# Kernel tuning notes

Hardware: AMD Instinct MI355X
Metric: run time of the kernel (lower is better)

Reference implementation:

```python
import jax, jax.numpy as jnp
import numpy as np

D_QK = 32  # out_channels // 8


def conv1x1(x, w, b):
    # x: [B,C,H,W], w: [O,C], b: [O] -> [B,O,H,W]
    return jnp.einsum('bchw,oc->bohw', x, w) + b[None, :, None, None]


def setup_inputs() -> dict:
    key = jax.random.key(0)
    ks = jax.random.split(key, 10)
    B, C, H, W = 4, 256, 64, 64
    in_ch, out_ch, attn_ch = 512, 256, 256
    s_in = 1.0 / np.sqrt(in_ch)
    s_at = 1.0 / np.sqrt(attn_ch)
    return {
        'ef': jax.random.normal(ks[0], (B, C, H, W), jnp.float32),
        'sf': jax.random.normal(ks[1], (B, C, H, W), jnp.float32),
        'Attn': jax.random.normal(ks[2], (B, attn_ch, H, W), jnp.float32),
        'Qw': jax.random.uniform(ks[3], (D_QK, in_ch), jnp.float32, -s_in, s_in),
        'Qb': jax.random.uniform(ks[4], (D_QK,), jnp.float32, -s_in, s_in),
        'Kw': jax.random.uniform(ks[5], (D_QK, attn_ch), jnp.float32, -s_at, s_at),
        'Kb': jax.random.uniform(ks[6], (D_QK,), jnp.float32, -s_at, s_at),
        'Vw': jax.random.uniform(ks[7], (out_ch, in_ch), jnp.float32, -s_in, s_in),
        'Vb': jax.random.uniform(ks[8], (out_ch,), jnp.float32, -s_in, s_in),
        'gamma': jnp.ones((1,), jnp.float32) * 0.25,
    }


def reference(ef, sf, Attn, Qw, Qb, Kw, Kb, Vw, Vb, gamma):
    B, C, H, W = ef.shape
    N = H * W
    x = jnp.concatenate((ef, sf), axis=1)  # [B, 2C, H, W]
    q = conv1x1(x, Qw, Qb).reshape(B, D_QK, N)         # [B, d, N]
    k = conv1x1(Attn, Kw, Kb).reshape(B, D_QK, N)      # [B, d, N]
    # scores[b, m, n] = sum_d q[b, d, m] * k[b, d, n]  (no 1/sqrt(d) scale)
    scores = jnp.einsum('bdm,bdn->bmn', q, k)
    attn = jax.nn.softmax(scores, axis=-1)             # [B, N, N]
    v = conv1x1(x, Vw, Vb).reshape(B, C, N)            # [B, C, N]
    # out[b, c, m] = sum_n v[b, c, n] * attn[b, m, n]
    out = jnp.einsum('bcn,bmn->bcm', v, attn).reshape(B, C, H, W)
    return gamma[0] * out + ef
```

## Files before the change

### kernel.cpp

```cpp
#include <hip/hip_runtime.h>
#include <hip/hip_bf16.h>

typedef short bf16x8 __attribute__((ext_vector_type(8)));
typedef float f32x4 __attribute__((ext_vector_type(4)));

#define MFMA16(a, b, c) __builtin_amdgcn_mfma_f32_16x16x32_bf16(a, b, c, 0, 0, 0)

#define NB 4
#define NC 256
#define NSP 4096
#define LOG2E 1.4426950408889634f

__device__ __forceinline__ unsigned short f2bf(float f) {
    return (unsigned short)((__float_as_uint(f) + 0x8000u) >> 16);
}
__device__ __forceinline__ unsigned pk2bf(float hi, float lo) {
    return __builtin_amdgcn_perm(__float_as_uint(hi) + 0x8000u,
                                 __float_as_uint(lo) + 0x8000u, 0x07060302u);
}

__global__ __launch_bounds__(256) void prep_w(
    const float* __restrict__ Qw, const float* __restrict__ Kw,
    const float* __restrict__ Vw,
    unsigned short* __restrict__ Qwbf, unsigned short* __restrict__ Kwbf,
    unsigned short* __restrict__ Vwbf)
{
    int i = blockIdx.x * 256 + threadIdx.x;
    {
        const float4* vs = (const float4*)(Vw + (size_t)i * 8);
        float4 a = vs[0], c = vs[1];
        int4 st;
        st.x = (int)pk2bf(a.y, a.x); st.y = (int)pk2bf(a.w, a.z);
        st.z = (int)pk2bf(c.y, c.x); st.w = (int)pk2bf(c.w, c.z);
        *(int4*)(Vwbf + (size_t)i * 8) = st;
    }
    if (i < 2048) {
        const float4* qs = (const float4*)(Qw + (size_t)i * 8);
        float4 a = qs[0], c = qs[1];
        int4 st;
        st.x = (int)pk2bf(a.y, a.x); st.y = (int)pk2bf(a.w, a.z);
        st.z = (int)pk2bf(c.y, c.x); st.w = (int)pk2bf(c.w, c.z);
        *(int4*)(Qwbf + (size_t)i * 8) = st;
    }
    if (i < 1024) {
        const float4* ks = (const float4*)(Kw + (size_t)i * 8);
        float4 a = ks[0], c = ks[1];
        int4 st;
        st.x = (int)pk2bf(a.y, a.x); st.y = (int)pk2bf(a.w, a.z);
        st.z = (int)pk2bf(c.y, c.x); st.w = (int)pk2bf(c.w, c.z);
        *(int4*)(Kwbf + (size_t)i * 8) = st;
    }
}

__global__ __launch_bounds__(256, 2) void proj_qv(
    const float* __restrict__ ef, const float* __restrict__ sf,
    const unsigned short* __restrict__ Qwbf, const float* __restrict__ Qb,
    const unsigned short* __restrict__ Vwbf, const float* __restrict__ Vb,
    unsigned short* __restrict__ qws, unsigned short* __restrict__ vws)
{
    __shared__ __align__(16) unsigned short xt[2][32][72];

    int t = threadIdx.x;
    int w = t >> 6, lane = t & 63, quad = lane >> 4, l15 = lane & 15;
    int mt = blockIdx.x, b = blockIdx.y, m0 = mt * 32;
    int u = t & 7, v = t >> 3;
    int mi = w >> 1, oh = w & 1;

    float4 xA[8], xB[8];
#pragma unroll
    for (int c = 0; c < 8; ++c) {
        const float* sp = (c < 4 ? ef : sf) +
                          ((size_t)(b * NC) + (c & 3) * 64 + 2 * v) * NSP + m0 + u * 4;
        xA[c] = *(const float4*)sp;
        xB[c] = *(const float4*)(sp + NSP);
    }

    f32x4 zero = {0.f, 0.f, 0.f, 0.f};
    f32x4 acc[2][4];
#pragma unroll
    for (int m = 0; m < 2; ++m)
#pragma unroll
        for (int ot = 0; ot < 4; ++ot) acc[m][ot] = zero;
    f32x4 qacc = zero;

#pragma unroll
    for (int c = 0; c < 8; ++c) {
        unsigned* xw = (unsigned*)&xt[c & 1][u * 4][2 * v];
        xw[0]   = pk2bf(xB[c].x, xA[c].x);
        xw[36]  = pk2bf(xB[c].y, xA[c].y);
        xw[72]  = pk2bf(xB[c].z, xA[c].z);
        xw[108] = pk2bf(xB[c].w, xA[c].w);
        __syncthreads();
        int ci0 = c * 64;
#pragma unroll
        for (int ks = 0; ks < 2; ++ks) {
            bf16x8 a0 = *(const bf16x8*)&xt[c & 1][l15][ks * 32 + quad * 8];
            bf16x8 a1 = *(const bf16x8*)&xt[c & 1][16 + l15][ks * 32 + quad * 8];
            bf16x8 bq = *(const bf16x8*)(Qwbf + (size_t)(oh * 16 + l15) * 512 + ci0 + ks * 32 + quad * 8);
            qacc = MFMA16(mi ? a1 : a0, bq, qacc);
#pragma unroll
            for (int ot = 0; ot < 4; ++ot) {
                bf16x8 bv = *(const bf16x8*)(Vwbf + (size_t)(w * 64 + ot * 16 + l15) * 512 + ci0 + ks * 32 + quad * 8);
                acc[0][ot] = MFMA16(a0, bv, acc[0][ot]);
                acc[1][ot] = MFMA16(a1, bv, acc[1][ot]);
            }
        }
    }

#pragma unroll
    for (int ot = 0; ot < 4; ++ot) {
        int ch = w * 64 + ot * 16 + l15;
        float bias = Vb[ch];
        unsigned* vp = (unsigned*)(vws + ((size_t)((b * 128 + mt) * 256 + ch)) * 32);
#pragma unroll
        for (int r = 0; r < 4; ++r)
            vp[quad * 4 + r] = pk2bf(acc[1][ot][r] + bias, acc[0][ot][r] + bias);
    }

    {
        int o = oh * 16 + l15;
        float bb = Qb[o];
#pragma unroll
        for (int r = 0; r < 4; ++r) {
            int m = m0 + mi * 16 + quad * 4 + r;
            qws[((size_t)(b * NSP) + m) * 32 + o] = f2bf((qacc[r] + bb) * LOG2E);
        }
    }
}

__global__ __launch_bounds__(256, 2) void proj_k(
    const float* __restrict__ attn,
    const unsigned short* __restrict__ Kwbf, const float* __restrict__ Kb,
    unsigned short* __restrict__ kws)
{
    __shared__ __align__(16) unsigned short xt[2][32][72];

    int t = threadIdx.x;
    int w = t >> 6, lane = t & 63, quad = lane >> 4, l15 = lane & 15;
    int mt = blockIdx.x, b = blockIdx.y, m0 = mt * 32;
    int u = t & 7, v = t >> 3;
    int mi = w >> 1, oh = w & 1;

    float4 xA[4], xB[4];
#pragma unroll
    for (int c = 0; c < 4; ++c) {
        const float* sp = attn + ((size_t)(b * NC) + c * 64 + 2 * v) * NSP + m0 + u * 4;
        xA[c] = *(const float4*)sp;
        xB[c] = *(const float4*)(sp + NSP);
    }

    f32x4 acc = {0.f, 0.f, 0.f, 0.f};

#pragma unroll
    for (int c = 0; c < 4; ++c) {
        unsigned* xw = (unsigned*)&xt[c & 1][u * 4][2 * v];
        xw[0]   = pk2bf(xB[c].x, xA[c].x);
        xw[36]  = pk2bf(xB[c].y, xA[c].y);
        xw[72]  = pk2bf(xB[c].z, xA[c].z);
        xw[108] = pk2bf(xB[c].w, xA[c].w);
        __syncthreads();
        int ci0 = c * 64;
#pragma unroll
        for (int ks = 0; ks < 2; ++ks) {
            bf16x8 a  = *(const bf16x8*)&xt[c & 1][mi * 16 + l15][ks * 32 + quad * 8];
            bf16x8 bk = *(const bf16x8*)(Kwbf + (size_t)(oh * 16 + l15) * 256 + ci0 + ks * 32 + quad * 8);
            acc = MFMA16(a, bk, acc);
        }
    }

    int o = oh * 16 + l15;
    float bb = Kb[o];
#pragma unroll
    for (int r = 0; r < 4; ++r) {
        int m = m0 + mi * 16 + quad * 4 + r;
        kws[((size_t)(b * NSP) + m) * 32 + o] = f2bf(acc[r] + bb);
    }
}

#define ATT_ITER(IT, VCUR, VNXT)                                              \
    {                                                                         \
        int buf = (IT) & 1;                                                   \
        f32x4 s0 = MFMA16(qf, kf[0], zero);                                   \
        f32x4 s1 = MFMA16(qf, kf[1], zero);                                   \
        f32x4 s2 = MFMA16(qf, kf[2], zero);                                   \
        f32x4 s3 = MFMA16(qf, kf[3], zero);                                   \
        float e0[4], e1[4], e2[4], e3[4];                                     \
        _Pragma("unroll")                                                     \
        for (int r = 0; r < 4; ++r) {                                         \
            e0[r] = __builtin_amdgcn_exp2f(s0[r]);                            \
            e1[r] = __builtin_amdgcn_exp2f(s1[r]);                            \
            e2[r] = __builtin_amdgcn_exp2f(s2[r]);                            \
            e3[r] = __builtin_amdgcn_exp2f(s3[r]);                            \
        }                                                                     \
        lp0 += (e0[0] + e1[0]) + (e2[0] + e3[0]);                             \
        lp1 += (e0[1] + e1[1]) + (e2[1] + e3[1]);                             \
        lp2 += (e0[2] + e1[2]) + (e2[2] + e3[2]);                             \
        lp3 += (e0[3] + e1[3]) + (e2[3] + e3[3]);                             \
        unsigned short* pd = &Plds[g][buf][(w * 16 + quad * 4) * 72 + 2 * l15]; \
        _Pragma("unroll")                                                     \
        for (int r = 0; r < 4; ++r) {                                         \
            *(unsigned*)(pd + r * 72)      = pk2bf(e1[r], e0[r]);             \
            *(unsigned*)(pd + r * 72 + 32) = pk2bf(e3[r], e2[r]);             \
        }                                                                     \
        int itn = (IT) + 1 < 32 ? (IT) + 1 : 31;                              \
        int ttn = tt0 + 2 * itn;                                              \
        _Pragma("unroll")                                                     \
        for (int j = 0; j < 4; ++j)                                           \
            kf[j] = *(const bf16x8*)(kbase + (size_t)((ttn + (j >> 1)) * 32 + (j & 1) * 16 + l15) * 32 + quad * 8); \
        _Pragma("unroll")                                                     \
        for (int h = 0; h < 2; ++h)                                           \
            _Pragma("unroll")                                                 \
            for (int cc = 0; cc < 4; ++cc)                                    \
                VNXT[h][cc] = *(const bf16x8*)(vbase + (size_t)(ttn + h) * 8192 + (w * 64 + cc * 16 + l15) * 32 + quad * 8); \
        __syncthreads();                                                      \
        _Pragma("unroll")                                                     \
        for (int h = 0; h < 2; ++h) {                                         \
            bf16x8 pa0 = *(const bf16x8*)&Plds[g][buf][(0  + l15) * 72 + h * 32 + quad * 8]; \
            bf16x8 pa1 = *(const bf16x8*)&Plds[g][buf][(16 + l15) * 72 + h * 32 + quad * 8]; \
            bf16x8 pa2 = *(const bf16x8*)&Plds[g][buf][(32 + l15) * 72 + h * 32 + quad * 8]; \
            bf16x8 pa3 = *(const bf16x8*)&Plds[g][buf][(48 + l15) * 72 + h * 32 + quad * 8]; \
            _Pragma("unroll")                                                 \
            for (int cc = 0; cc < 4; ++cc) {                                  \
                acc[0][cc] = MFMA16(pa0, VCUR[h][cc], acc[0][cc]);            \
                acc[1][cc] = MFMA16(pa1, VCUR[h][cc], acc[1][cc]);            \
                acc[2][cc] = MFMA16(pa2, VCUR[h][cc], acc[2][cc]);            \
                acc[3][cc] = MFMA16(pa3, VCUR[h][cc], acc[3][cc]);            \
            }                                                                 \
        }                                                                     \
    }

__global__ __launch_bounds__(512, 2) void attention(
    const unsigned short* __restrict__ qws, const unsigned short* __restrict__ kws,
    const unsigned short* __restrict__ vws, const float* __restrict__ ef,
    const float* __restrict__ gamma, float* __restrict__ out)
{
    __shared__ unsigned short Plds[2][2][64 * 72];
    __shared__ float mrg[256][68];
    __shared__ float denl[2][64];

    int t = threadIdx.x;
    int g = t >> 8, tl = t & 255;
    int w = tl >> 6, lane = tl & 63, quad = lane >> 4, l15 = lane & 15;
    int b = blockIdx.x >> 6, m0 = (blockIdx.x & 63) << 6;

    const unsigned short* kbase = kws + (size_t)(b * NSP) * 32;
    const unsigned short* vbase = vws + (size_t)(b * 128) * 8192;

    bf16x8 qf = *(const bf16x8*)(qws + ((size_t)(b * NSP) + m0 + w * 16 + l15) * 32 + quad * 8);

    f32x4 zero = {0.f, 0.f, 0.f, 0.f};
    f32x4 acc[4][4];
#pragma unroll
    for (int i = 0; i < 4; ++i)
#pragma unroll
        for (int j = 0; j < 4; ++j) acc[i][j] = zero;
    float lp0 = 0.f, lp1 = 0.f, lp2 = 0.f, lp3 = 0.f;

    int tt0 = g * 64;
    bf16x8 kf[4];
#pragma unroll
    for (int j = 0; j < 4; ++j)
        kf[j] = *(const bf16x8*)(kbase + (size_t)((tt0 + (j >> 1)) * 32 + (j & 1) * 16 + l15) * 32 + quad * 8);
    bf16x8 vfA[2][4], vfB[2][4];
#pragma unroll
    for (int h = 0; h < 2; ++h)
#pragma unroll
        for (int cc = 0; cc < 4; ++cc)
            vfA[h][cc] = *(const bf16x8*)(vbase + (size_t)(tt0 + h) * 8192 + (w * 64 + cc * 16 + l15) * 32 + quad * 8);

    for (int it2 = 0; it2 < 16; ++it2) {
        ATT_ITER(2 * it2,     vfA, vfB);
        ATT_ITER(2 * it2 + 1, vfB, vfA);
    }

    lp0 += __shfl_xor(lp0, 1); lp0 += __shfl_xor(lp0, 2); lp0 += __shfl_xor(lp0, 4); lp0 += __shfl_xor(lp0, 8);
    lp1 += __shfl_xor(lp1, 1); lp1 += __shfl_xor(lp1, 2); lp1 += __shfl_xor(lp1, 4); lp1 += __shfl_xor(lp1, 8);
    lp2 += __shfl_xor(lp2, 1); lp2 += __shfl_xor(lp2, 2); lp2 += __shfl_xor(lp2, 4); lp2 += __shfl_xor(lp2, 8);
    lp3 += __shfl_xor(lp3, 1); lp3 += __shfl_xor(lp3, 2); lp3 += __shfl_xor(lp3, 4); lp3 += __shfl_xor(lp3, 8);
    if (l15 == 0) {
        int base = w * 16 + quad * 4;
        denl[g][base + 0] = lp0; denl[g][base + 1] = lp1;
        denl[g][base + 2] = lp2; denl[g][base + 3] = lp3;
    }
    if (g == 1) {
#pragma unroll
        for (int qc = 0; qc < 4; ++qc)
#pragma unroll
            for (int cc = 0; cc < 4; ++cc)
                *(f32x4*)&mrg[w * 64 + cc * 16 + l15][qc * 16 + quad * 4] = acc[qc][cc];
    }
    __syncthreads();

    if (g == 0) {
        float gam = gamma[0];
#pragma unroll
        for (int qc = 0; qc < 4; ++qc) {
            int qb = qc * 16 + quad * 4;
            float4 d0 = *(const float4*)&denl[0][qb];
            float4 d1 = *(const float4*)&denl[1][qb];
            float r0 = gam / (d0.x + d1.x), r1 = gam / (d0.y + d1.y);
            float r2 = gam / (d0.z + d1.z), r3 = gam / (d0.w + d1.w);
#pragma unroll
            for (int cc = 0; cc < 4; ++cc) {
                int ch = w * 64 + cc * 16 + l15;
                f32x4 part = *(const f32x4*)&mrg[ch][qb];
                size_t off = ((size_t)(b * NC + ch)) * NSP + m0 + qb;
                float4 e = *(const float4*)(ef + off);
                float4 o;
                o.x = (acc[qc][cc][0] + part[0]) * r0 + e.x;
                o.y = (acc[qc][cc][1] + part[1]) * r1 + e.y;
                o.z = (acc[qc][cc][2] + part[2]) * r2 + e.z;
                o.w = (acc[qc][cc][3] + part[3]) * r3 + e.w;
                *(float4*)(out + off) = o;
            }
        }
    }
}

extern "C" void kernel_launch(void* const* d_in, const int* in_sizes, int n_in,
                              void* d_out, int out_size, void* d_ws, size_t ws_size,
                              hipStream_t stream) {
    const float* ef    = (const float*)d_in[0];
    const float* sf    = (const float*)d_in[1];
    const float* attn  = (const float*)d_in[2];
    const float* Qw    = (const float*)d_in[3];
    const float* Qb    = (const float*)d_in[4];
    const float* Kw    = (const float*)d_in[5];
    const float* Kb    = (const float*)d_in[6];
    const float* Vw    = (const float*)d_in[7];
    const float* Vb    = (const float*)d_in[8];
    const float* gamma = (const float*)d_in[9];
    float* out = (float*)d_out;

    unsigned short* qws  = (unsigned short*)d_ws;
    unsigned short* kws  = qws + (size_t)4 * 4096 * 32;
    unsigned short* vws  = kws + (size_t)4 * 4096 * 32;
    unsigned short* Qwbf = vws + (size_t)4 * 128 * 256 * 32;
    unsigned short* Kwbf = Qwbf + 32 * 512;
    unsigned short* Vwbf = Kwbf + 32 * 256;

    hipLaunchKernelGGL(prep_w, dim3(64), dim3(256), 0, stream,
                       Qw, Kw, Vw, Qwbf, Kwbf, Vwbf);
    hipLaunchKernelGGL(proj_qv, dim3(128, 4), dim3(256), 0, stream,
                       ef, sf, Qwbf, Qb, Vwbf, Vb, qws, vws);
    hipLaunchKernelGGL(proj_k, dim3(128, 4), dim3(256), 0, stream,
                       attn, Kwbf, Kb, kws);
    hipLaunchKernelGGL(attention, dim3(256), dim3(512), 0, stream,
                       qws, kws, vws, ef, gamma, out);
}
```

Measured before the change: 179.8 us.

## Split attention key range into separate blocks with global merge kernel

Replaces the single 512-thread attention kernel, which split the key range between two thread groups inside one block and merged through shared memory, with 512 independent 256-thread blocks that each handle half of the keys. Each block writes unnormalised partial outputs and denominators to global memory, and a new elementwise kernel sums the two halves, normalises, applies gamma and adds the residual. This aims to raise occupancy and drop the large shared-memory merge buffer. In exchange it adds about 16 MB of extra global traffic and one more launch. Scheduling barriers are also added after the input loads in the projection kernels.

```diff
diff --git a/kernel.cpp b/kernel.cpp
--- a/kernel.cpp
+++ b/kernel.cpp
@@ -74,6 +74,7 @@
         xA[c] = *(const float4*)sp;
         xB[c] = *(const float4*)(sp + NSP);
     }
+    __builtin_amdgcn_sched_barrier(0);
 
     f32x4 zero = {0.f, 0.f, 0.f, 0.f};
     f32x4 acc[2][4];
@@ -116,7 +117,6 @@
         for (int r = 0; r < 4; ++r)
             vp[quad * 4 + r] = pk2bf(acc[1][ot][r] + bias, acc[0][ot][r] + bias);
     }
-
     {
         int o = oh * 16 + l15;
         float bb = Qb[o];
@@ -148,6 +148,7 @@
         xA[c] = *(const float4*)sp;
         xB[c] = *(const float4*)(sp + NSP);
     }
+    __builtin_amdgcn_sched_barrier(0);
 
     f32x4 acc = {0.f, 0.f, 0.f, 0.f};
 
@@ -175,6 +176,148 @@
         int m = m0 + mi * 16 + quad * 4 + r;
         kws[((size_t)(b * NSP) + m) * 32 + o] = f2bf(acc[r] + bb);
     }
+}
+
+#define ATT_ITER_P(IT, VCUR, VNXT)                                            \
+    {                                                                         \
+        int buf = (IT) & 1;                                                   \
+        f32x4 s0 = MFMA16(qf, kf[0], zero);                                   \
+        f32x4 s1 = MFMA16(qf, kf[1], zero);                                   \
+        f32x4 s2 = MFMA16(qf, kf[2], zero);                                   \
+        f32x4 s3 = MFMA16(qf, kf[3], zero);                                   \
+        float e0[4], e1[4], e2[4], e3[4];                                     \
+        _Pragma("unroll")                                                     \
+        for (int r = 0; r < 4; ++r) {                                         \
+            e0[r] = __builtin_amdgcn_exp2f(s0[r]);                            \
+            e1[r] = __builtin_amdgcn_exp2f(s1[r]);                            \
+            e2[r] = __builtin_amdgcn_exp2f(s2[r]);                            \
+            e3[r] = __builtin_amdgcn_exp2f(s3[r]);                            \
+        }                                                                     \
+        lp0 += (e0[0] + e1[0]) + (e2[0] + e3[0]);                             \
+        lp1 += (e0[1] + e1[1]) + (e2[1] + e3[1]);                             \
+        lp2 += (e0[2] + e1[2]) + (e2[2] + e3[2]);                             \
+        lp3 += (e0[3] + e1[3]) + (e2[3] + e3[3]);                             \
+        unsigned short* pd = &Plds[buf][(w * 16 + quad * 4) * 72 + 2 * l15];  \
+        _Pragma("unroll")                                                     \
+        for (int r = 0; r < 4; ++r) {                                         \
+            *(unsigned*)(pd + r * 72)      = pk2bf(e1[r], e0[r]);             \
+            *(unsigned*)(pd + r * 72 + 32) = pk2bf(e3[r], e2[r]);             \
+        }                                                                     \
+        int itn = (IT) + 1 < 32 ? (IT) + 1 : 31;                              \
+        int ttn = tt0 + 2 * itn;                                              \
+        _Pragma("unroll")                                                     \
+        for (int j = 0; j < 4; ++j)                                           \
+            kf[j] = *(const bf16x8*)(kbase + (size_t)((ttn + (j >> 1)) * 32 + (j & 1) * 16 + l15) * 32 + quad * 8); \
+        _Pragma("unroll")                                                     \
+        for (int h = 0; h < 2; ++h)                                           \
+            _Pragma("unroll")                                                 \
+            for (int cc = 0; cc < 4; ++cc)                                    \
+                VNXT[h][cc] = *(const bf16x8*)(vbase + (size_t)(ttn + h) * 8192 + (w * 64 + cc * 16 + l15) * 32 + quad * 8); \
+        __syncthreads();                                                      \
+        _Pragma("unroll")                                                     \
+        for (int h = 0; h < 2; ++h) {                                         \
+            bf16x8 pa0 = *(const bf16x8*)&Plds[buf][(0  + l15) * 72 + h * 32 + quad * 8]; \
+            bf16x8 pa1 = *(const bf16x8*)&Plds[buf][(16 + l15) * 72 + h * 32 + quad * 8]; \
+            bf16x8 pa2 = *(const bf16x8*)&Plds[buf][(32 + l15) * 72 + h * 32 + quad * 8]; \
+            bf16x8 pa3 = *(const bf16x8*)&Plds[buf][(48 + l15) * 72 + h * 32 + quad * 8]; \
+            _Pragma("unroll")                                                 \
+            for (int cc = 0; cc < 4; ++cc) {                                  \
+                acc[0][cc] = MFMA16(pa0, VCUR[h][cc], acc[0][cc]);            \
+                acc[1][cc] = MFMA16(pa1, VCUR[h][cc], acc[1][cc]);            \
+                acc[2][cc] = MFMA16(pa2, VCUR[h][cc], acc[2][cc]);            \
+                acc[3][cc] = MFMA16(pa3, VCUR[h][cc], acc[3][cc]);            \
+            }                                                                 \
+        }                                                                     \
+    }
+
+__global__ __launch_bounds__(256, 2) void attention_part(
+    const unsigned short* __restrict__ qws, const unsigned short* __restrict__ kws,
+    const unsigned short* __restrict__ vws,
+    float* __restrict__ opart0, float* __restrict__ opart1,
+    float* __restrict__ denp)
+{
+    __shared__ unsigned short Plds[2][64 * 72];
+
+    int t = threadIdx.x;
+    int w = t >> 6, lane = t & 63, quad = lane >> 4, l15 = lane & 15;
+    int bx = blockIdx.x;
+    int g = bx & 1;
+    int r2 = bx >> 1;
+    int b = r2 >> 6, m0 = (r2 & 63) << 6;
+
+    const unsigned short* kbase = kws + (size_t)(b * NSP) * 32;
+    const unsigned short* vbase = vws + (size_t)(b * 128) * 8192;
+
+    bf16x8 qf = *(const bf16x8*)(qws + ((size_t)(b * NSP) + m0 + w * 16 + l15) * 32 + quad * 8);
+
+    f32x4 zero = {0.f, 0.f, 0.f, 0.f};
+    f32x4 acc[4][4];
+#pragma unroll
+    for (int i = 0; i < 4; ++i)
+#pragma unroll
+        for (int j = 0; j < 4; ++j) acc[i][j] = zero;
+    float lp0 = 0.f, lp1 = 0.f, lp2 = 0.f, lp3 = 0.f;
+
+    int tt0 = g * 64;
+    bf16x8 kf[4];
+#pragma unroll
+    for (int j = 0; j < 4; ++j)
+        kf[j] = *(const bf16x8*)(kbase + (size_t)((tt0 + (j >> 1)) * 32 + (j & 1) * 16 + l15) * 32 + quad * 8);
+    bf16x8 vfA[2][4], vfB[2][4];
+#pragma unroll
+    for (int h = 0; h < 2; ++h)
+#pragma unroll
+        for (int cc = 0; cc < 4; ++cc)
+            vfA[h][cc] = *(const bf16x8*)(vbase + (size_t)(tt0 + h) * 8192 + (w * 64 + cc * 16 + l15) * 32 + quad * 8);
+
+    for (int it2 = 0; it2 < 16; ++it2) {
+        ATT_ITER_P(2 * it2,     vfA, vfB);
+        ATT_ITER_P(2 * it2 + 1, vfB, vfA);
+    }
+
+    lp0 += __shfl_xor(lp0, 1); lp0 += __shfl_xor(lp0, 2); lp0 += __shfl_xor(lp0, 4); lp0 += __shfl_xor(lp0, 8);
+    lp1 += __shfl_xor(lp1, 1); lp1 += __shfl_xor(lp1, 2); lp1 += __shfl_xor(lp1, 4); lp1 += __shfl_xor(lp1, 8);
+    lp2 += __shfl_xor(lp2, 1); lp2 += __shfl_xor(lp2, 2); lp2 += __shfl_xor(lp2, 4); lp2 += __shfl_xor(lp2, 8);
+    lp3 += __shfl_xor(lp3, 1); lp3 += __shfl_xor(lp3, 2); lp3 += __shfl_xor(lp3, 4); lp3 += __shfl_xor(lp3, 8);
+    if (l15 == 0) {
+        float* dp = denp + ((size_t)(g * 4 + b)) * NSP + m0 + w * 16 + quad * 4;
+        dp[0] = lp0; dp[1] = lp1; dp[2] = lp2; dp[3] = lp3;
+    }
+
+    float* od = g ? opart1 : opart0;
+#pragma unroll
+    for (int qc = 0; qc < 4; ++qc) {
+#pragma unroll
+        for (int cc = 0; cc < 4; ++cc) {
+            int ch = w * 64 + cc * 16 + l15;
+            size_t off = ((size_t)(b * NC + ch)) * NSP + m0 + qc * 16 + quad * 4;
+            *(f32x4*)(od + off) = acc[qc][cc];
+        }
+    }
+}
+
+__global__ __launch_bounds__(256) void attn_merge(
+    const float* __restrict__ o1, const float* __restrict__ denp,
+    const float* __restrict__ ef, const float* __restrict__ gamma,
+    float* __restrict__ out)
+{
+    size_t i = (size_t)blockIdx.x * 256 + threadIdx.x;
+    size_t off = i * 4;
+    int m = (int)(off & (NSP - 1));
+    int b = (int)(i >> 18);
+
+    float4 a0 = *(const float4*)(out + off);
+    float4 a1 = *(const float4*)(o1 + off);
+    float4 d0 = *(const float4*)(denp + ((size_t)(0 * 4 + b)) * NSP + m);
+    float4 d1 = *(const float4*)(denp + ((size_t)(1 * 4 + b)) * NSP + m);
+    float4 e  = *(const float4*)(ef + off);
+    float gam = gamma[0];
+    float4 o;
+    o.x = (a0.x + a1.x) * (gam / (d0.x + d1.x)) + e.x;
+    o.y = (a0.y + a1.y) * (gam / (d0.y + d1.y)) + e.y;
+    o.z = (a0.z + a1.z) * (gam / (d0.z + d1.z)) + e.z;
+    o.w = (a0.w + a1.w) * (gam / (d0.w + d1.w)) + e.w;
+    *(float4*)(out + off) = o;
 }
 
 #define ATT_ITER(IT, VCUR, VNXT)                                              \
@@ -229,7 +372,7 @@
         }                                                                     \
     }
 
-__global__ __launch_bounds__(512, 2) void attention(
+__global__ __launch_bounds__(512, 2) void attention_fb(
     const unsigned short* __restrict__ qws, const unsigned short* __restrict__ kws,
     const unsigned short* __restrict__ vws, const float* __restrict__ ef,
     const float* __restrict__ gamma, float* __restrict__ out)
@@ -338,6 +481,10 @@
     unsigned short* Qwbf = vws + (size_t)4 * 128 * 256 * 32;
     unsigned short* Kwbf = Qwbf + 32 * 512;
     unsigned short* Vwbf = Kwbf + 32 * 256;
+    unsigned short* wend = Vwbf + 256 * 512;
+    float* o1ws = (float*)(((((size_t)(wend - (unsigned short*)d_ws)) * 2 + 255) & ~(size_t)255) / 1 + (char*)d_ws);
+    float* denp = o1ws + (size_t)NB * NC * NSP;
+    size_t need = ((char*)(denp + 2 * NB * NSP)) - (char*)d_ws;
 
     hipLaunchKernelGGL(prep_w, dim3(64), dim3(256), 0, stream,
                        Qw, Kw, Vw, Qwbf, Kwbf, Vwbf);
@@ -345,6 +492,13 @@
                        ef, sf, Qwbf, Qb, Vwbf, Vb, qws, vws);
     hipLaunchKernelGGL(proj_k, dim3(128, 4), dim3(256), 0, stream,
                        attn, Kwbf, Kb, kws);
-    hipLaunchKernelGGL(attention, dim3(256), dim3(512), 0, stream,
-                       qws, kws, vws, ef, gamma, out);
-}
+    if (ws_size >= need) {
+        hipLaunchKernelGGL(attention_part, dim3(512), dim3(256), 0, stream,
+                           qws, kws, vws, out, o1ws, denp);
+        hipLaunchKernelGGL(attn_merge, dim3(4096), dim3(256), 0, stream,
+                           o1ws, denp, ef, gamma, out);
+    } else {
+        hipLaunchKernelGGL(attention_fb, dim3(256), dim3(512), 0, stream,
+                           qws, kws, vws, ef, gamma, out);
+    }
+}
```

Result: slower. 191.7 us (+6.6%).

## Prefetch projection weights one chunk ahead and remap attention block order

Applied to the files above, without the earlier changes.

In the Q/V and K projection kernels, weight fragments for the next input-channel chunk are loaded into double-buffered registers while the current chunk's MFMAs run, and sched barriers keep the compiler from reordering those loads. This hides global-load latency for weights that were previously fetched inline with the MFMAs, at the cost of more live registers. The attention kernel also permutes blockIdx so that consecutive block IDs are spread across batches and tiles, presumably to match the mi355x's per-XCD round-robin block dispatch and improve cache locality of K/V.

```diff
diff --git a/kernel.cpp b/kernel.cpp
--- a/kernel.cpp
+++ b/kernel.cpp
@@ -74,6 +74,22 @@
         xA[c] = *(const float4*)sp;
         xB[c] = *(const float4*)(sp + NSP);
     }
+    __builtin_amdgcn_sched_barrier(0);
+
+    const unsigned short* qwp = Qwbf + (size_t)(oh * 16 + l15) * 512 + quad * 8;
+    const unsigned short* vwp[4];
+#pragma unroll
+    for (int ot = 0; ot < 4; ++ot)
+        vwp[ot] = Vwbf + (size_t)(w * 64 + ot * 16 + l15) * 512 + quad * 8;
+
+    bf16x8 wq[2][2], wv[2][2][4];
+#pragma unroll
+    for (int ks = 0; ks < 2; ++ks) {
+        wq[0][ks] = *(const bf16x8*)(qwp + ks * 32);
+#pragma unroll
+        for (int ot = 0; ot < 4; ++ot)
+            wv[0][ks][ot] = *(const bf16x8*)(vwp[ot] + ks * 32);
+    }
 
     f32x4 zero = {0.f, 0.f, 0.f, 0.f};
     f32x4 acc[2][4];
@@ -85,24 +101,35 @@
 
 #pragma unroll
     for (int c = 0; c < 8; ++c) {
-        unsigned* xw = (unsigned*)&xt[c & 1][u * 4][2 * v];
+        int cur = c & 1, nxt = cur ^ 1;
+        unsigned* xw = (unsigned*)&xt[cur][u * 4][2 * v];
         xw[0]   = pk2bf(xB[c].x, xA[c].x);
         xw[36]  = pk2bf(xB[c].y, xA[c].y);
         xw[72]  = pk2bf(xB[c].z, xA[c].z);
         xw[108] = pk2bf(xB[c].w, xA[c].w);
         __syncthreads();
-        int ci0 = c * 64;
+
+        if (c < 7) {
+            int ci0n = (c + 1) * 64;
+#pragma unroll
+            for (int ks = 0; ks < 2; ++ks) {
+                wq[nxt][ks] = *(const bf16x8*)(qwp + ci0n + ks * 32);
+#pragma unroll
+                for (int ot = 0; ot < 4; ++ot)
+                    wv[nxt][ks][ot] = *(const bf16x8*)(vwp[ot] + ci0n + ks * 32);
+            }
+        }
+        __builtin_amdgcn_sched_barrier(0);
+
 #pragma unroll
         for (int ks = 0; ks < 2; ++ks) {
-            bf16x8 a0 = *(const bf16x8*)&xt[c & 1][l15][ks * 32 + quad * 8];
-            bf16x8 a1 = *(const bf16x8*)&xt[c & 1][16 + l15][ks * 32 + quad * 8];
-            bf16x8 bq = *(const bf16x8*)(Qwbf + (size_t)(oh * 16 + l15) * 512 + ci0 + ks * 32 + quad * 8);
-            qacc = MFMA16(mi ? a1 : a0, bq, qacc);
+            bf16x8 a0 = *(const bf16x8*)&xt[cur][l15][ks * 32 + quad * 8];
+            bf16x8 a1 = *(const bf16x8*)&xt[cur][16 + l15][ks * 32 + quad * 8];
+            qacc = MFMA16(mi ? a1 : a0, wq[cur][ks], qacc);
 #pragma unroll
             for (int ot = 0; ot < 4; ++ot) {
-                bf16x8 bv = *(const bf16x8*)(Vwbf + (size_t)(w * 64 + ot * 16 + l15) * 512 + ci0 + ks * 32 + quad * 8);
-                acc[0][ot] = MFMA16(a0, bv, acc[0][ot]);
-                acc[1][ot] = MFMA16(a1, bv, acc[1][ot]);
+                acc[0][ot] = MFMA16(a0, wv[cur][ks][ot], acc[0][ot]);
+                acc[1][ot] = MFMA16(a1, wv[cur][ks][ot], acc[1][ot]);
             }
         }
     }
@@ -116,7 +143,6 @@
         for (int r = 0; r < 4; ++r)
             vp[quad * 4 + r] = pk2bf(acc[1][ot][r] + bias, acc[0][ot][r] + bias);
     }
-
     {
         int o = oh * 16 + l15;
         float bb = Qb[o];
@@ -148,23 +174,38 @@
         xA[c] = *(const float4*)sp;
         xB[c] = *(const float4*)(sp + NSP);
     }
+    __builtin_amdgcn_sched_barrier(0);
+
+    const unsigned short* kwp = Kwbf + (size_t)(oh * 16 + l15) * 256 + quad * 8;
+    bf16x8 wk[2][2];
+#pragma unroll
+    for (int ks = 0; ks < 2; ++ks)
+        wk[0][ks] = *(const bf16x8*)(kwp + ks * 32);
 
     f32x4 acc = {0.f, 0.f, 0.f, 0.f};
 
 #pragma unroll
     for (int c = 0; c < 4; ++c) {
-        unsigned* xw = (unsigned*)&xt[c & 1][u * 4][2 * v];
+        int cur = c & 1, nxt = cur ^ 1;
+        unsigned* xw = (unsigned*)&xt[cur][u * 4][2 * v];
         xw[0]   = pk2bf(xB[c].x, xA[c].x);
         xw[36]  = pk2bf(xB[c].y, xA[c].y);
         xw[72]  = pk2bf(xB[c].z, xA[c].z);
         xw[108] = pk2bf(xB[c].w, xA[c].w);
         __syncthreads();
-        int ci0 = c * 64;
+
+        if (c < 3) {
+            int ci0n = (c + 1) * 64;
+#pragma unroll
+            for (int ks = 0; ks < 2; ++ks)
+                wk[nxt][ks] = *(const bf16x8*)(kwp + ci0n + ks * 32);
+        }
+        __builtin_amdgcn_sched_barrier(0);
+
 #pragma unroll
         for (int ks = 0; ks < 2; ++ks) {
-            bf16x8 a  = *(const bf16x8*)&xt[c & 1][mi * 16 + l15][ks * 32 + quad * 8];
-            bf16x8 bk = *(const bf16x8*)(Kwbf + (size_t)(oh * 16 + l15) * 256 + ci0 + ks * 32 + quad * 8);
-            acc = MFMA16(a, bk, acc);
+            bf16x8 a = *(const bf16x8*)&xt[cur][mi * 16 + l15][ks * 32 + quad * 8];
+            acc = MFMA16(a, wk[cur][ks], acc);
         }
     }
 
@@ -241,7 +282,8 @@
     int t = threadIdx.x;
     int g = t >> 8, tl = t & 255;
     int w = tl >> 6, lane = tl & 63, quad = lane >> 4, l15 = lane & 15;
-    int b = blockIdx.x >> 6, m0 = (blockIdx.x & 63) << 6;
+    int bs = (blockIdx.x & 7) * 32 + (blockIdx.x >> 3);
+    int b = bs >> 6, m0 = (bs & 63) << 6;
 
     const unsigned short* kbase = kws + (size_t)(b * NSP) * 32;
     const unsigned short* vbase = vws + (size_t)(b * 128) * 8192;
```

New measurement: 180.0 us. No clear change (+0.1%).
